# Optimization experiments

Measured on AMD Instinct MI355X. Metric: run time of the kernel, lower is better.

Reference implementation:

```python
import jax, jax.numpy as jnp
from jax import lax
import numpy as np

NUM_BINS = 4
GROUPS = 196
PS = 16  # patch_size
CH = 3 * GROUPS  # 588


def quick_gelu(x):
    return x * jax.nn.sigmoid(1.702 * x)


def avgpool3_exclude_pad(x):
    # AvgPool2d(kernel=3, stride=1, padding=1, count_include_pad=False)
    win = (1, 1, 3, 3)
    strides = (1, 1, 1, 1)
    pad = ((0, 0), (0, 0), (1, 1), (1, 1))
    s = lax.reduce_window(x, jnp.float32(0.0), lax.add, win, strides, pad)
    ones = jnp.ones((1, 1) + x.shape[-2:], x.dtype)
    cnt = lax.reduce_window(ones, jnp.float32(0.0), lax.add, win, strides, pad)
    return s / cnt


def setup_inputs() -> dict:
    key = jax.random.key(0)
    ks = jax.random.split(key, 6)
    B = 64
    x = jax.random.normal(ks[0], (B, 197, 768), jnp.float32)
    # adapter_conv: Conv2d(588,588,3,groups=196) -> OIHW weight [588,3,3,3]
    conv_w = jax.random.normal(ks[1], (CH, 3, 3, 3), jnp.float32) * (1.0 / np.sqrt(27.0))
    conv_b = jnp.zeros((CH,), jnp.float32)
    # HistogramLayer: bin_centers_conv.bias (learnable), bin_widths_conv.weight (learnable)
    centers = jax.random.normal(ks[2], (NUM_BINS * CH,), jnp.float32) * 0.1
    widths = jax.random.normal(ks[3], (NUM_BINS * CH,), jnp.float32) * 0.1 + 1.0
    # adapter_conv_down: Conv2d(2352,588,1,groups=196) -> per-group [3 out, 12 in]
    down_w = jax.random.normal(ks[4], (GROUPS, 3, 12), jnp.float32) * 0.1
    down_b = jax.random.normal(ks[5], (CH,), jnp.float32) * 0.1
    return dict(x=x, conv_w=conv_w, conv_b=conv_b, centers=centers,
                widths=widths, down_w=down_w, down_b=down_b)


def reference(x, conv_w, conv_b, centers, widths, down_w, down_b):
    B, N, C = x.shape  # (64, 197, 768)
    x_cls = x[:, :1, :]
    xp = x[:, 1:, :].reshape(B, (N - 1) * 3, PS, PS)  # (B, 588, 16, 16)

    # grouped 3x3 conv, groups=196 (3->3 per group)
    y = lax.conv_general_dilated(
        xp, conv_w, window_strides=(1, 1), padding=((1, 1), (1, 1)),
        dimension_numbers=('NCHW', 'OIHW', 'NCHW'), feature_group_count=GROUPS)
    y = y + conv_b[None, :, None, None]
    y = quick_gelu(y)

    # HistogramLayer: bin_centers (weight frozen at 1) -> abs; bin_widths (bias frozen at 1) -> relu
    h = jnp.abs(jnp.repeat(y, NUM_BINS, axis=1) + centers[None, :, None, None])  # (B, 2352, 16, 16)
    h = jax.nn.relu(widths[None, :, None, None] * h + 1.0)

    # constrain_bins: per-(channel-group of 4 bins) sum-normalize
    Bn, Cn, H, W = h.shape
    hr = h.reshape(Bn, Cn // NUM_BINS, NUM_BINS, H, W)
    h = (hr / (hr.sum(axis=2, keepdims=True) + 1e-5)).reshape(Bn, Cn, H, W)

    # normalize_count: AvgPool2d(3, stride=1, pad=1, count_include_pad=False)
    h = avgpool3_exclude_pad(h)
    h = quick_gelu(h)

    # adapter_conv_down: grouped 1x1 conv, 12 -> 3 per group of 196
    hg = h.reshape(B, GROUPS, 12, H, W)
    o = jnp.einsum('bgihw,goi->bgohw', hg, down_w) + down_b.reshape(1, GROUPS, 3, 1, 1)
    o = o.reshape(B, GROUPS, 768)  # (3*16*16 = 768 per patch token)

    return jnp.concatenate([x_cls, o], axis=1)  # (B, 197, 768)
```

## Files before the change

kernel.cpp:

```cpp
#include <hip/hip_runtime.h>

#define GROUPS 196

__device__ __forceinline__ float dppL(float v) {
    return __int_as_float(__builtin_amdgcn_update_dpp(
        __float_as_int(v), __float_as_int(v), 0x111, 0xF, 0xF, true));
}
__device__ __forceinline__ float dppR(float v) {
    return __int_as_float(__builtin_amdgcn_update_dpp(
        __float_as_int(v), __float_as_int(v), 0x101, 0xF, 0xF, true));
}
__device__ __forceinline__ float bperm(int addr, float v) {
    return __int_as_float(__builtin_amdgcn_ds_bpermute(addr, __float_as_int(v)));
}
__device__ __forceinline__ float qgelu(float v) {
    return v * __builtin_amdgcn_rcpf(1.0f + __expf(-1.702f * v));
}
__device__ __forceinline__ float qgelu01(float p) {
    return p * fmaf(p, fmaf(p, -0.11333f, 0.46195f), 0.49805f);
}

__global__ __launch_bounds__(256) void convpass_fused(
    const float* __restrict__ x,
    const float* __restrict__ conv_w,
    const float* __restrict__ conv_b,
    const float* __restrict__ centers,
    const float* __restrict__ widths,
    const float* __restrict__ down_w,
    const float* __restrict__ down_b,
    float* __restrict__ out)
{
    const int tid = threadIdx.x;
    const int l  = tid & 63;
    const int wv = tid >> 6;
    const int g  = blockIdx.x * 4 + wv;
    const int b  = blockIdx.y;
    const int q  = l >> 4;
    const int py = l & 15;
    const float mL = (q > 0) ? 1.f : 0.f;
    const float mR = (q < 3) ? 1.f : 0.f;
    const int aL = ((l - 16) & 63) << 2;
    const int aR = ((l + 16) & 63) << 2;

    const int sg = __builtin_amdgcn_readfirstlane(g);
    const float* cw  = conv_w  + sg * 81;
    const float* cen = centers + sg * 12;
    const float* wid = widths  + sg * 12;
    const float* dwp = down_w  + sg * 36;

    const int tok = b * 197 + g + 1;
    const float4* xin4 = (const float4*)x + tok * 192;
    const int fo = py * 4 + q;
    float4 A0 = xin4[fo];
    float4 A1 = xin4[64 + fo];
    float4 A2 = xin4[128 + fo];

    float acc[3][4];
    {
        const float cb0 = conv_b[sg*3+0], cb1 = conv_b[sg*3+1], cb2 = conv_b[sg*3+2];
        #pragma unroll
        for (int j = 0; j < 4; ++j) { acc[0][j] = cb0; acc[1][j] = cb1; acc[2][j] = cb2; }
    }
    #pragma unroll
    for (int ic = 0; ic < 3; ++ic) {
        const float4 a = (ic == 0) ? A0 : (ic == 1) ? A1 : A2;
        const float eL = bperm(aL, a.w) * mL;
        const float eR = bperm(aR, a.x) * mR;
        #pragma unroll
        for (int ky = 0; ky < 3; ++ky) {
            float4 v; float vl, vr;
            if (ky == 0)      { v = make_float4(dppL(a.x), dppL(a.y), dppL(a.z), dppL(a.w));
                                vl = dppL(eL); vr = dppL(eR); }
            else if (ky == 1) { v = a; vl = eL; vr = eR; }
            else              { v = make_float4(dppR(a.x), dppR(a.y), dppR(a.z), dppR(a.w));
                                vl = dppR(eL); vr = dppR(eR); }
            #pragma unroll
            for (int oc = 0; oc < 3; ++oc) {
                const float w0 = cw[oc*27 + ic*9 + ky*3 + 0];
                const float w1 = cw[oc*27 + ic*9 + ky*3 + 1];
                const float w2 = cw[oc*27 + ic*9 + ky*3 + 2];
                acc[oc][0] = fmaf(vl,  w0, fmaf(v.x, w1, fmaf(v.y, w2, acc[oc][0])));
                acc[oc][1] = fmaf(v.x, w0, fmaf(v.y, w1, fmaf(v.z, w2, acc[oc][1])));
                acc[oc][2] = fmaf(v.y, w0, fmaf(v.z, w1, fmaf(v.w, w2, acc[oc][2])));
                acc[oc][3] = fmaf(v.z, w0, fmaf(v.w, w1, fmaf(vr,  w2, acc[oc][3])));
            }
        }
    }

    const bool  vy2 = (py == 0) | (py == 15);
    const float rE = vy2 ? 0.25f     : (1.f/6.f);
    const float rM = vy2 ? (1.f/6.f) : (1.f/9.f);
    const float rc0 = (q == 0) ? rE : rM;
    const float rc3 = (q == 3) ? rE : rM;

    float o[3][4];
    {
        const float db0 = down_b[sg*3+0], db1 = down_b[sg*3+1], db2 = down_b[sg*3+2];
        #pragma unroll
        for (int j = 0; j < 4; ++j) { o[0][j] = db0; o[1][j] = db1; o[2][j] = db2; }
    }

    #pragma unroll
    for (int oc = 0; oc < 3; ++oc) {
        float hj[3][4];
        #pragma unroll
        for (int j = 0; j < 4; ++j) {
            const float y = qgelu(acc[oc][j]);
            const float t0 = fmaf(wid[oc*4+0], fabsf(y + cen[oc*4+0]), 1.0f);
            const float t1 = fmaf(wid[oc*4+1], fabsf(y + cen[oc*4+1]), 1.0f);
            const float t2 = fmaf(wid[oc*4+2], fabsf(y + cen[oc*4+2]), 1.0f);
            const float t3 = fmaf(wid[oc*4+3], fabsf(y + cen[oc*4+3]), 1.0f);
            const float inv = __builtin_amdgcn_rcpf((t0 + t1) + (t2 + t3));
            hj[0][j] = t0 * inv; hj[1][j] = t1 * inv; hj[2][j] = t2 * inv;
        }
        float rs[3][4];
        #pragma unroll
        for (int k = 0; k < 3; ++k) {
            const float lh = bperm(aL, hj[k][3]);
            const float rh = bperm(aR, hj[k][0]);
            const float s01 = hj[k][0] + hj[k][1];
            const float s23 = hj[k][2] + hj[k][3];
            rs[k][0] = fmaf(mL, lh, s01);
            rs[k][1] = s01 + hj[k][2];
            rs[k][2] = hj[k][1] + s23;
            rs[k][3] = fmaf(mR, rh, s23);
        }
        #pragma unroll
        for (int j = 0; j < 4; ++j) {
            const float rcj = (j == 0) ? rc0 : (j == 3) ? rc3 : rM;
            const float v0 = rs[0][j] + dppL(rs[0][j]) + dppR(rs[0][j]);
            const float v1 = rs[1][j] + dppL(rs[1][j]) + dppR(rs[1][j]);
            const float v2 = rs[2][j] + dppL(rs[2][j]) + dppR(rs[2][j]);
            const float p0 = v0 * rcj;
            const float p1 = v1 * rcj;
            const float p2 = v2 * rcj;
            const float p3 = 1.0f - p0 - p1 - p2;
            const float u0 = qgelu01(p0);
            const float u1 = qgelu01(p1);
            const float u2 = qgelu01(p2);
            const float u3 = qgelu01(p3);
            const int i = oc * 4;
            o[0][j] = fmaf(u0, dwp[i],    fmaf(u1, dwp[i+1],    fmaf(u2, dwp[i+2],    fmaf(u3, dwp[i+3],    o[0][j]))));
            o[1][j] = fmaf(u0, dwp[12+i], fmaf(u1, dwp[12+i+1], fmaf(u2, dwp[12+i+2], fmaf(u3, dwp[12+i+3], o[1][j]))));
            o[2][j] = fmaf(u0, dwp[24+i], fmaf(u1, dwp[24+i+1], fmaf(u2, dwp[24+i+2], fmaf(u3, dwp[24+i+3], o[2][j]))));
        }
    }

    float4* op4 = (float4*)out + tok * 192;
    op4[fo]       = make_float4(o[0][0], o[0][1], o[0][2], o[0][3]);
    op4[64 + fo]  = make_float4(o[1][0], o[1][1], o[1][2], o[1][3]);
    op4[128 + fo] = make_float4(o[2][0], o[2][1], o[2][2], o[2][3]);

    if (g == 0) {
        const float4* xc = (const float4*)x + b * 197 * 192;
        float4* oc4 = (float4*)out + b * 197 * 192;
        oc4[l]       = xc[l];
        oc4[64 + l]  = xc[64 + l];
        oc4[128 + l] = xc[128 + l];
    }
}

extern "C" void kernel_launch(void* const* d_in, const int* in_sizes, int n_in,
                              void* d_out, int out_size, void* d_ws, size_t ws_size,
                              hipStream_t stream) {
    const float* x       = (const float*)d_in[0];
    const float* conv_w  = (const float*)d_in[1];
    const float* conv_b  = (const float*)d_in[2];
    const float* centers = (const float*)d_in[3];
    const float* widths  = (const float*)d_in[4];
    const float* down_w  = (const float*)d_in[5];
    const float* down_b  = (const float*)d_in[6];
    float* out = (float*)d_out;

    const int B = in_sizes[0] / (197 * 768);

    dim3 grid(GROUPS / 4, B);
    convpass_fused<<<grid, 256, 0, stream>>>(x, conv_w, conv_b, centers, widths,
                                             down_w, down_b, out);
}
```

Baseline: 31.37 us.

## Process four batch items per block with software-prefetched input loads

Each block now loops over four batch elements, reusing the per-group weights, biases and histogram parameters loaded once, and prefetches the next batch element's input tile while computing the current one. The grid shrinks by a factor of four in the batch dimension. This amortizes parameter loads and hides global load latency, but cuts the block count to 784, which lowers parallelism and occupancy-based latency hiding, and it assumes B is divisible by four.

Result: slower. 50.00 us (+59.4%).

```diff
diff --git a/kernel.cpp b/kernel.cpp
--- a/kernel.cpp
+++ b/kernel.cpp
@@ -34,7 +34,7 @@
     const int l  = tid & 63;
     const int wv = tid >> 6;
     const int g  = blockIdx.x * 4 + wv;
-    const int b  = blockIdx.y;
+    const int b0 = blockIdx.y * 4;
     const int q  = l >> 4;
     const int py = l & 15;
     const float mL = (q > 0) ? 1.f : 0.f;
@@ -47,45 +47,8 @@
     const float* cen = centers + sg * 12;
     const float* wid = widths  + sg * 12;
     const float* dwp = down_w  + sg * 36;
-
-    const int tok = b * 197 + g + 1;
-    const float4* xin4 = (const float4*)x + tok * 192;
-    const int fo = py * 4 + q;
-    float4 A0 = xin4[fo];
-    float4 A1 = xin4[64 + fo];
-    float4 A2 = xin4[128 + fo];
-
-    float acc[3][4];
-    {
-        const float cb0 = conv_b[sg*3+0], cb1 = conv_b[sg*3+1], cb2 = conv_b[sg*3+2];
-        #pragma unroll
-        for (int j = 0; j < 4; ++j) { acc[0][j] = cb0; acc[1][j] = cb1; acc[2][j] = cb2; }
-    }
-    #pragma unroll
-    for (int ic = 0; ic < 3; ++ic) {
-        const float4 a = (ic == 0) ? A0 : (ic == 1) ? A1 : A2;
-        const float eL = bperm(aL, a.w) * mL;
-        const float eR = bperm(aR, a.x) * mR;
-        #pragma unroll
-        for (int ky = 0; ky < 3; ++ky) {
-            float4 v; float vl, vr;
-            if (ky == 0)      { v = make_float4(dppL(a.x), dppL(a.y), dppL(a.z), dppL(a.w));
-                                vl = dppL(eL); vr = dppL(eR); }
-            else if (ky == 1) { v = a; vl = eL; vr = eR; }
-            else              { v = make_float4(dppR(a.x), dppR(a.y), dppR(a.z), dppR(a.w));
-                                vl = dppR(eL); vr = dppR(eR); }
-            #pragma unroll
-            for (int oc = 0; oc < 3; ++oc) {
-                const float w0 = cw[oc*27 + ic*9 + ky*3 + 0];
-                const float w1 = cw[oc*27 + ic*9 + ky*3 + 1];
-                const float w2 = cw[oc*27 + ic*9 + ky*3 + 2];
-                acc[oc][0] = fmaf(vl,  w0, fmaf(v.x, w1, fmaf(v.y, w2, acc[oc][0])));
-                acc[oc][1] = fmaf(v.x, w0, fmaf(v.y, w1, fmaf(v.z, w2, acc[oc][1])));
-                acc[oc][2] = fmaf(v.y, w0, fmaf(v.z, w1, fmaf(v.w, w2, acc[oc][2])));
-                acc[oc][3] = fmaf(v.z, w0, fmaf(v.w, w1, fmaf(vr,  w2, acc[oc][3])));
-            }
-        }
-    }
+    const float cb0 = conv_b[sg*3+0], cb1 = conv_b[sg*3+1], cb2 = conv_b[sg*3+2];
+    const float db0 = down_b[sg*3+0], db1 = down_b[sg*3+1], db2 = down_b[sg*3+2];
 
     const bool  vy2 = (py == 0) | (py == 15);
     const float rE = vy2 ? 0.25f     : (1.f/6.f);
@@ -93,70 +56,116 @@
     const float rc0 = (q == 0) ? rE : rM;
     const float rc3 = (q == 3) ? rE : rM;
 
-    float o[3][4];
-    {
-        const float db0 = down_b[sg*3+0], db1 = down_b[sg*3+1], db2 = down_b[sg*3+2];
+    const int fo = py * 4 + q;
+    const float4* xb = (const float4*)x + ((size_t)b0 * 197 + g + 1) * 192;
+    float4 A0 = xb[fo];
+    float4 A1 = xb[64 + fo];
+    float4 A2 = xb[128 + fo];
+
+    #pragma unroll 1
+    for (int i = 0; i < 4; ++i) {
+        float4 N0 = A0, N1 = A1, N2 = A2;
+        if (i < 3) {
+            const float4* xn = xb + (size_t)(i + 1) * (197 * 192);
+            N0 = xn[fo]; N1 = xn[64 + fo]; N2 = xn[128 + fo];
+        }
+
+        float acc[3][4];
+        #pragma unroll
+        for (int j = 0; j < 4; ++j) { acc[0][j] = cb0; acc[1][j] = cb1; acc[2][j] = cb2; }
+        #pragma unroll
+        for (int ic = 0; ic < 3; ++ic) {
+            const float4 a = (ic == 0) ? A0 : (ic == 1) ? A1 : A2;
+            const float eL = bperm(aL, a.w) * mL;
+            const float eR = bperm(aR, a.x) * mR;
+            #pragma unroll
+            for (int ky = 0; ky < 3; ++ky) {
+                float4 v; float vl, vr;
+                if (ky == 0)      { v = make_float4(dppL(a.x), dppL(a.y), dppL(a.z), dppL(a.w));
+                                    vl = dppL(eL); vr = dppL(eR); }
+                else if (ky == 1) { v = a; vl = eL; vr = eR; }
+                else              { v = make_float4(dppR(a.x), dppR(a.y), dppR(a.z), dppR(a.w));
+                                    vl = dppR(eL); vr = dppR(eR); }
+                #pragma unroll
+                for (int oc = 0; oc < 3; ++oc) {
+                    const float w0 = cw[oc*27 + ic*9 + ky*3 + 0];
+                    const float w1 = cw[oc*27 + ic*9 + ky*3 + 1];
+                    const float w2 = cw[oc*27 + ic*9 + ky*3 + 2];
+                    acc[oc][0] = fmaf(vl,  w0, fmaf(v.x, w1, fmaf(v.y, w2, acc[oc][0])));
+                    acc[oc][1] = fmaf(v.x, w0, fmaf(v.y, w1, fmaf(v.z, w2, acc[oc][1])));
+                    acc[oc][2] = fmaf(v.y, w0, fmaf(v.z, w1, fmaf(v.w, w2, acc[oc][2])));
+                    acc[oc][3] = fmaf(v.z, w0, fmaf(v.w, w1, fmaf(vr,  w2, acc[oc][3])));
+                }
+            }
+        }
+
+        float o[3][4];
         #pragma unroll
         for (int j = 0; j < 4; ++j) { o[0][j] = db0; o[1][j] = db1; o[2][j] = db2; }
+
+        #pragma unroll
+        for (int oc = 0; oc < 3; ++oc) {
+            float hj[3][4];
+            #pragma unroll
+            for (int j = 0; j < 4; ++j) {
+                const float y = qgelu(acc[oc][j]);
+                const float t0 = fmaf(wid[oc*4+0], fabsf(y + cen[oc*4+0]), 1.0f);
+                const float t1 = fmaf(wid[oc*4+1], fabsf(y + cen[oc*4+1]), 1.0f);
+                const float t2 = fmaf(wid[oc*4+2], fabsf(y + cen[oc*4+2]), 1.0f);
+                const float t3 = fmaf(wid[oc*4+3], fabsf(y + cen[oc*4+3]), 1.0f);
+                const float inv = __builtin_amdgcn_rcpf((t0 + t1) + (t2 + t3));
+                hj[0][j] = t0 * inv; hj[1][j] = t1 * inv; hj[2][j] = t2 * inv;
+            }
+            float rs[3][4];
+            #pragma unroll
+            for (int k = 0; k < 3; ++k) {
+                const float lh = bperm(aL, hj[k][3]);
+                const float rh = bperm(aR, hj[k][0]);
+                const float s01 = hj[k][0] + hj[k][1];
+                const float s23 = hj[k][2] + hj[k][3];
+                rs[k][0] = fmaf(mL, lh, s01);
+                rs[k][1] = s01 + hj[k][2];
+                rs[k][2] = hj[k][1] + s23;
+                rs[k][3] = fmaf(mR, rh, s23);
+            }
+            #pragma unroll
+            for (int j = 0; j < 4; ++j) {
+                const float rcj = (j == 0) ? rc0 : (j == 3) ? rc3 : rM;
+                const float v0 = rs[0][j] + dppL(rs[0][j]) + dppR(rs[0][j]);
+                const float v1 = rs[1][j] + dppL(rs[1][j]) + dppR(rs[1][j]);
+                const float v2 = rs[2][j] + dppL(rs[2][j]) + dppR(rs[2][j]);
+                const float p0 = v0 * rcj;
+                const float p1 = v1 * rcj;
+                const float p2 = v2 * rcj;
+                const float p3 = 1.0f - p0 - p1 - p2;
+                const float u0 = qgelu01(p0);
+                const float u1 = qgelu01(p1);
+                const float u2 = qgelu01(p2);
+                const float u3 = qgelu01(p3);
+                const int ii = oc * 4;
+                o[0][j] = fmaf(u0, dwp[ii],    fmaf(u1, dwp[ii+1],    fmaf(u2, dwp[ii+2],    fmaf(u3, dwp[ii+3],    o[0][j]))));
+                o[1][j] = fmaf(u0, dwp[12+ii], fmaf(u1, dwp[12+ii+1], fmaf(u2, dwp[12+ii+2], fmaf(u3, dwp[12+ii+3], o[1][j]))));
+                o[2][j] = fmaf(u0, dwp[24+ii], fmaf(u1, dwp[24+ii+1], fmaf(u2, dwp[24+ii+2], fmaf(u3, dwp[24+ii+3], o[2][j]))));
+            }
+        }
+
+        float4* op4 = (float4*)out + ((size_t)(b0 + i) * 197 + g + 1) * 192;
+        op4[fo]       = make_float4(o[0][0], o[0][1], o[0][2], o[0][3]);
+        op4[64 + fo]  = make_float4(o[1][0], o[1][1], o[1][2], o[1][3]);
+        op4[128 + fo] = make_float4(o[2][0], o[2][1], o[2][2], o[2][3]);
+
+        A0 = N0; A1 = N1; A2 = N2;
     }
 
-    #pragma unroll
-    for (int oc = 0; oc < 3; ++oc) {
-        float hj[3][4];
-        #pragma unroll
-        for (int j = 0; j < 4; ++j) {
-            const float y = qgelu(acc[oc][j]);
-            const float t0 = fmaf(wid[oc*4+0], fabsf(y + cen[oc*4+0]), 1.0f);
-            const float t1 = fmaf(wid[oc*4+1], fabsf(y + cen[oc*4+1]), 1.0f);
-            const float t2 = fmaf(wid[oc*4+2], fabsf(y + cen[oc*4+2]), 1.0f);
-            const float t3 = fmaf(wid[oc*4+3], fabsf(y + cen[oc*4+3]), 1.0f);
-            const float inv = __builtin_amdgcn_rcpf((t0 + t1) + (t2 + t3));
-            hj[0][j] = t0 * inv; hj[1][j] = t1 * inv; hj[2][j] = t2 * inv;
+    if (g == 0) {
+        #pragma unroll 1
+        for (int i = 0; i < 4; ++i) {
+            const float4* xc = (const float4*)x + (size_t)(b0 + i) * 197 * 192;
+            float4* oc4 = (float4*)out + (size_t)(b0 + i) * 197 * 192;
+            oc4[l]       = xc[l];
+            oc4[64 + l]  = xc[64 + l];
+            oc4[128 + l] = xc[128 + l];
         }
-        float rs[3][4];
-        #pragma unroll
-        for (int k = 0; k < 3; ++k) {
-            const float lh = bperm(aL, hj[k][3]);
-            const float rh = bperm(aR, hj[k][0]);
-            const float s01 = hj[k][0] + hj[k][1];
-            const float s23 = hj[k][2] + hj[k][3];
-            rs[k][0] = fmaf(mL, lh, s01);
-            rs[k][1] = s01 + hj[k][2];
-            rs[k][2] = hj[k][1] + s23;
-            rs[k][3] = fmaf(mR, rh, s23);
-        }
-        #pragma unroll
-        for (int j = 0; j < 4; ++j) {
-            const float rcj = (j == 0) ? rc0 : (j == 3) ? rc3 : rM;
-            const float v0 = rs[0][j] + dppL(rs[0][j]) + dppR(rs[0][j]);
-            const float v1 = rs[1][j] + dppL(rs[1][j]) + dppR(rs[1][j]);
-            const float v2 = rs[2][j] + dppL(rs[2][j]) + dppR(rs[2][j]);
-            const float p0 = v0 * rcj;
-            const float p1 = v1 * rcj;
-            const float p2 = v2 * rcj;
-            const float p3 = 1.0f - p0 - p1 - p2;
-            const float u0 = qgelu01(p0);
-            const float u1 = qgelu01(p1);
-            const float u2 = qgelu01(p2);
-            const float u3 = qgelu01(p3);
-            const int i = oc * 4;
-            o[0][j] = fmaf(u0, dwp[i],    fmaf(u1, dwp[i+1],    fmaf(u2, dwp[i+2],    fmaf(u3, dwp[i+3],    o[0][j]))));
-            o[1][j] = fmaf(u0, dwp[12+i], fmaf(u1, dwp[12+i+1], fmaf(u2, dwp[12+i+2], fmaf(u3, dwp[12+i+3], o[1][j]))));
-            o[2][j] = fmaf(u0, dwp[24+i], fmaf(u1, dwp[24+i+1], fmaf(u2, dwp[24+i+2], fmaf(u3, dwp[24+i+3], o[2][j]))));
-        }
-    }
-
-    float4* op4 = (float4*)out + tok * 192;
-    op4[fo]       = make_float4(o[0][0], o[0][1], o[0][2], o[0][3]);
-    op4[64 + fo]  = make_float4(o[1][0], o[1][1], o[1][2], o[1][3]);
-    op4[128 + fo] = make_float4(o[2][0], o[2][1], o[2][2], o[2][3]);
-
-    if (g == 0) {
-        const float4* xc = (const float4*)x + b * 197 * 192;
-        float4* oc4 = (float4*)out + b * 197 * 192;
-        oc4[l]       = xc[l];
-        oc4[64 + l]  = xc[64 + l];
-        oc4[128 + l] = xc[128 + l];
     }
 }
 
@@ -174,7 +183,7 @@
 
     const int B = in_sizes[0] / (197 * 768);
 
-    dim3 grid(GROUPS / 4, B);
+    dim3 grid(GROUPS / 4, B / 4);
     convpass_fused<<<grid, 256, 0, stream>>>(x, conv_w, conv_b, centers, widths,
                                              down_w, down_b, out);
 }
```
